# Optimization experiments

Measured on AMD Instinct MI355X. Metric: run time of the kernel, lower is better.

Reference implementation:

```python
import jax, jax.numpy as jnp
import numpy as np

H, C, HID, L, NF, B = 4, 128, 128, 3, 5, 32  # heads, per-head dim, hidden, layers, node feats, graphs
LN_EPS = 1e-5


def setup_inputs() -> dict:
    key = jax.random.key(0)
    ks = jax.random.split(key, 12)
    N, E = 10000, 160000
    x = jax.random.normal(ks[0], (N, NF), dtype=jnp.float32)
    edge_index = jax.random.randint(ks[1], (2, E), 0, N, dtype=jnp.int64)
    batch = jnp.sort(jax.random.randint(ks[2], (N,), 0, B, dtype=jnp.int64))
    s = 0.1
    return {
        "x": x,
        "edge_index": edge_index,
        "batch": batch,
        "node_W": jax.random.normal(ks[3], (NF, HID), dtype=jnp.float32) * s,
        "node_b": jnp.zeros((HID,), dtype=jnp.float32),
        "Ws": jax.random.normal(ks[4], (L, HID, H * C), dtype=jnp.float32) * s,
        "att_srcs": jax.random.normal(ks[5], (L, H, C), dtype=jnp.float32) * s,
        "att_dsts": jax.random.normal(ks[6], (L, H, C), dtype=jnp.float32) * s,
        "biases": jnp.zeros((L, HID), dtype=jnp.float32),
        "ln_gs": jnp.ones((L, HID), dtype=jnp.float32),
        "ln_bs": jnp.zeros((L, HID), dtype=jnp.float32),
    }


def _layer_norm(x, g, b):
    mu = jnp.mean(x, axis=-1, keepdims=True)
    var = jnp.mean(jnp.square(x - mu), axis=-1, keepdims=True)
    return (x - mu) * jax.lax.rsqrt(var + LN_EPS) * g + b


def _gat_layer(x, W, att_src, att_dst, bias, src, dst, N):
    # x: [N, HID]; PyG GATConv, heads=H, concat=False (mean over heads)
    h = (x @ W).reshape(N, H, C)                       # [N,H,C]
    a_src = jnp.sum(h * att_src, axis=-1)              # [N,H]
    a_dst = jnp.sum(h * att_dst, axis=-1)              # [N,H]
    e = jax.nn.leaky_relu(a_src[src] + a_dst[dst], 0.2)  # [E,H]
    # edge-softmax over destination neighborhoods (numerically stable)
    m = jax.ops.segment_max(e, dst, num_segments=N)
    ex = jnp.exp(e - m[dst])
    denom = jax.ops.segment_sum(ex, dst, num_segments=N)
    alpha = ex / (denom[dst] + 1e-16)                  # [E,H]
    msg = h[src] * alpha[:, :, None]                   # [E,H,C]
    out = jax.ops.segment_sum(msg, dst, num_segments=N)  # [N,H,C]
    return out.mean(axis=1) + bias                     # concat=False -> head mean


def reference(x, edge_index, batch, node_W, node_b, Ws, att_srcs, att_dsts,
              biases, ln_gs, ln_bs):
    N = x.shape[0]
    loop = jnp.arange(N, dtype=edge_index.dtype)
    src = jnp.concatenate([edge_index[0], loop])       # PyG adds self-loops
    dst = jnp.concatenate([edge_index[1], loop])

    h = jax.nn.relu(x @ node_W + node_b)               # [N,HID]
    for l in range(L):
        h_new = _gat_layer(h, Ws[l], att_srcs[l], att_dsts[l], biases[l], src, dst, N)
        h_new = _layer_norm(h_new, ln_gs[l], ln_bs[l])
        h = jax.nn.relu(h_new) + h                     # residual; dropout is identity in eval

    # global mean pool over graphs
    sums = jax.ops.segment_sum(h, batch, num_segments=B)
    cnts = jax.ops.segment_sum(jnp.ones((N, 1), h.dtype), batch, num_segments=B)
    graph_emb = sums / jnp.maximum(cnts, 1.0)
    return h, graph_emb
```

## Files before the change

### kernel.cpp

```cpp
#include <hip/hip_runtime.h>
#include <math.h>

#define N_NODES 10000
#define N_EDGES 160000
#define E2 (N_EDGES + N_NODES)
#define HIDDEN 128
#define NHEAD 4
#define NB 32
#define LN_EPS 1e-5f

typedef __attribute__((ext_vector_type(8))) short bf16x8;
typedef __attribute__((ext_vector_type(4))) float f32x4;

__device__ __forceinline__ unsigned short f2bf(float f) {
    unsigned int u = __float_as_uint(f);
    u += 0x7fffu + ((u >> 16) & 1u);
    return (unsigned short)(u >> 16);
}
__device__ __forceinline__ float bf2f_lo(unsigned int u) { return __uint_as_float(u << 16); }
__device__ __forceinline__ float bf2f_hi(unsigned int u) { return __uint_as_float(u & 0xffff0000u); }

__global__ void k_init(int* counts, int* gstart, int* gend, float* gout) {
    int i = blockIdx.x * blockDim.x + threadIdx.x;
    if (i < N_NODES) counts[i] = 1;
    if (i < NB) { gstart[i] = N_NODES; gend[i] = 0; }
    if (i < NB * HIDDEN) gout[i] = 0.f;
}

__global__ void k_hist(const int* __restrict__ ei, int* counts) {
    int e = blockIdx.x * blockDim.x + threadIdx.x;
    if (e < N_EDGES) atomicAdd(&counts[ei[N_EDGES + e]], 1);
}

__global__ void k_scan(const int* __restrict__ counts, int* rowptr, int* cursor) {
    __shared__ int sums[1024];
    int t = threadIdx.x;
    const int per = 10;
    int base = t * per;
    int loc[per];
    int s = 0;
    for (int i = 0; i < per; i++) {
        int idx = base + i;
        int v = (idx < N_NODES) ? counts[idx] : 0;
        loc[i] = s; s += v;
    }
    sums[t] = s;
    __syncthreads();
    for (int off = 1; off < 1024; off <<= 1) {
        int v = (t >= off) ? sums[t - off] : 0;
        __syncthreads();
        sums[t] += v;
        __syncthreads();
    }
    int prefix = (t > 0) ? sums[t - 1] : 0;
    for (int i = 0; i < per; i++) {
        int idx = base + i;
        if (idx < N_NODES) { int r = prefix + loc[i]; rowptr[idx] = r; cursor[idx] = r; }
    }
    if (t == 1023) rowptr[N_NODES] = sums[1023];
}

__global__ void k_scatter(const int* __restrict__ ei, int* cursor, int* csr_src) {
    int e = blockIdx.x * blockDim.x + threadIdx.x;
    if (e < N_EDGES) {
        int s = ei[e], d = ei[N_EDGES + e];
        int pos = atomicAdd(&cursor[d], 1);
        csr_src[pos] = s;
    } else if (e < E2) {
        int n = e - N_EDGES;
        int pos = atomicAdd(&cursor[n], 1);
        csr_src[pos] = n;
    }
}

__global__ void k_bounds(const int* __restrict__ batch, int* gstart, int* gend) {
    int n = blockIdx.x * blockDim.x + threadIdx.x;
    if (n >= N_NODES) return;
    int b = batch[n];
    if (n == 0 || batch[n - 1] != b) gstart[b] = n;
    if (n == N_NODES - 1 || batch[n + 1] != b) gend[b] = n + 1;
}

__global__ void k_convB(const float* __restrict__ Ws, unsigned short* __restrict__ Btb) {
    int t = blockIdx.x * blockDim.x + threadIdx.x;
    if (t >= 3 * 512 * 128) return;
    int l = t >> 16, rem = t & 65535;
    int n = rem >> 7, k = rem & 127;
    Btb[t] = f2bf(Ws[l * 65536 + k * 512 + n]);
}

__global__ void k_input(const float* __restrict__ x, const float* __restrict__ W,
                        const float* __restrict__ b, float* __restrict__ h,
                        unsigned short* __restrict__ hb) {
    int t = blockIdx.x * blockDim.x + threadIdx.x;
    if (t >= N_NODES * HIDDEN) return;
    int n = t >> 7, c = t & 127;
    float s = b[c];
    #pragma unroll
    for (int k = 0; k < 5; k++) s += x[n * 5 + k] * W[k * HIDDEN + c];
    float r = fmaxf(s, 0.f);
    h[t] = r;
    hb[t] = f2bf(r);
}

__global__ __launch_bounds__(256) void k_gemm(const unsigned short* __restrict__ Ab,
                                              const unsigned short* __restrict__ Bt,
                                              unsigned short* __restrict__ Cb) {
    int wave = threadIdx.x >> 6, lane = threadIdx.x & 63;
    int q = lane >> 4, u = lane & 15;
    int mbase = blockIdx.y * 64 + wave * 16;
    int nbase = blockIdx.x * 64;
    int arow = mbase + u;
    if (arow > N_NODES - 1) arow = N_NODES - 1;
    bf16x8 a[4];
    #pragma unroll
    for (int k0 = 0; k0 < 4; k0++)
        a[k0] = *(const bf16x8*)(Ab + (size_t)arow * 128 + k0 * 32 + q * 8);
    f32x4 acc[4];
    #pragma unroll
    for (int nb = 0; nb < 4; nb++) acc[nb] = (f32x4){0.f, 0.f, 0.f, 0.f};
    #pragma unroll
    for (int nb = 0; nb < 4; nb++) {
        const unsigned short* bp = Bt + (size_t)(nbase + nb * 16 + u) * 128 + q * 8;
        #pragma unroll
        for (int k0 = 0; k0 < 4; k0++) {
            bf16x8 bfr = *(const bf16x8*)(bp + k0 * 32);
            acc[nb] = __builtin_amdgcn_mfma_f32_16x16x32_bf16(a[k0], bfr, acc[nb], 0, 0, 0);
        }
    }
    #pragma unroll
    for (int nb = 0; nb < 4; nb++) {
        int col = nbase + nb * 16 + u;
        #pragma unroll
        for (int r = 0; r < 4; r++) {
            int row = mbase + q * 4 + r;
            if (row < N_NODES) Cb[(size_t)row * 512 + col] = f2bf(acc[nb][r]);
        }
    }
}

__global__ void k_att(const unsigned int* __restrict__ hb32,
                      const float* __restrict__ ws,
                      const float* __restrict__ wd, float* __restrict__ a_src,
                      float* __restrict__ a_dst) {
    int widx = blockIdx.x * 4 + (threadIdx.x >> 6);
    int lane = threadIdx.x & 63;
    if (widx >= N_NODES * NHEAD) return;
    int n = widx >> 2, h = widx & 3;
    unsigned int u = hb32[(size_t)n * 256 + h * 64 + lane];
    float v0 = bf2f_lo(u), v1 = bf2f_hi(u);
    int c = 2 * lane;
    float s = v0 * ws[h * 128 + c] + v1 * ws[h * 128 + c + 1];
    float d = v0 * wd[h * 128 + c] + v1 * wd[h * 128 + c + 1];
    #pragma unroll
    for (int o = 32; o > 0; o >>= 1) { s += __shfl_down(s, o); d += __shfl_down(d, o); }
    if (lane == 0) { a_src[widx] = s; a_dst[widx] = d; }
}

__global__ __launch_bounds__(256) void k_agg(const uint4* __restrict__ hb4,
                                             const int* __restrict__ rowptr,
                                             const int* __restrict__ csr,
                                             const float* __restrict__ a_src,
                                             const float* __restrict__ a_dst,
                                             const float* __restrict__ bias,
                                             const float* __restrict__ lng,
                                             const float* __restrict__ lnb,
                                             float* __restrict__ h,
                                             unsigned short* __restrict__ hbn) {
    int wave = threadIdx.x >> 6;
    int lane = threadIdx.x & 63;
    int n = blockIdx.x * 4 + wave;
    if (n >= N_NODES) return;
    int hl = lane >> 4;
    int pos = lane & 15;
    int off = rowptr[n];
    int deg = rowptr[n + 1] - off;
    float adn = a_dst[n * 4 + hl];
    float m = -INFINITY, denom = 0.f;
    float o[8] = {};
    for (int base = 0; base < deg; base += 64) {
        int cnt = min(64, deg - base);
        int s = (lane < cnt) ? csr[off + base + lane] : 0;
        for (int i = 0; i < cnt; i++) {
            int si = __shfl(s, i);
            float t = a_src[si * 4 + hl] + adn;
            float e = t > 0.f ? t : 0.2f * t;
            float nm = fmaxf(m, e);
            float sc = __expf(m - nm);
            float p = __expf(e - nm);
            denom = denom * sc + p;
            uint4 u = hb4[(size_t)si * 64 + lane];
            o[0] = o[0] * sc + p * bf2f_lo(u.x);
            o[1] = o[1] * sc + p * bf2f_hi(u.x);
            o[2] = o[2] * sc + p * bf2f_lo(u.y);
            o[3] = o[3] * sc + p * bf2f_hi(u.y);
            o[4] = o[4] * sc + p * bf2f_lo(u.z);
            o[5] = o[5] * sc + p * bf2f_hi(u.z);
            o[6] = o[6] * sc + p * bf2f_lo(u.w);
            o[7] = o[7] * sc + p * bf2f_hi(u.w);
            m = nm;
        }
    }
    float inv = 1.f / (denom + 1e-16f);
    #pragma unroll
    for (int k = 0; k < 8; k++) o[k] *= inv;
    #pragma unroll
    for (int k = 0; k < 8; k++) {
        o[k] += __shfl_xor(o[k], 16);
        o[k] += __shfl_xor(o[k], 32);
    }
    float v[8], sv = 0.f, sq = 0.f;
    #pragma unroll
    for (int k = 0; k < 8; k++) {
        float b = bias[8 * pos + k];
        v[k] = 0.25f * o[k] + b;
        sv += v[k]; sq += v[k] * v[k];
    }
    #pragma unroll
    for (int d = 8; d > 0; d >>= 1) {
        sv += __shfl_xor(sv, d);
        sq += __shfl_xor(sq, d);
    }
    float mu = sv * (1.f / 128.f);
    float var = sq * (1.f / 128.f) - mu * mu;
    float rs = rsqrtf(var + LN_EPS);
    if (hl == 0) {
        float* hrow = h + (size_t)n * 128 + 8 * pos;
        float4 old0 = *(const float4*)(hrow);
        float4 old1 = *(const float4*)(hrow + 4);
        float r[8];
        #pragma unroll
        for (int k = 0; k < 8; k++) {
            float y = (v[k] - mu) * rs * lng[8 * pos + k] + lnb[8 * pos + k];
            r[k] = fmaxf(y, 0.f);
        }
        float w[8] = {r[0] + old0.x, r[1] + old0.y, r[2] + old0.z, r[3] + old0.w,
                      r[4] + old1.x, r[5] + old1.y, r[6] + old1.z, r[7] + old1.w};
        *(float4*)(hrow) = make_float4(w[0], w[1], w[2], w[3]);
        *(float4*)(hrow + 4) = make_float4(w[4], w[5], w[6], w[7]);
        ushort4 p0, p1;
        p0.x = f2bf(w[0]); p0.y = f2bf(w[1]); p0.z = f2bf(w[2]); p0.w = f2bf(w[3]);
        p1.x = f2bf(w[4]); p1.y = f2bf(w[5]); p1.z = f2bf(w[6]); p1.w = f2bf(w[7]);
        unsigned short* hbrow = hbn + (size_t)n * 128 + 8 * pos;
        *(ushort4*)(hbrow) = p0;
        *(ushort4*)(hbrow + 4) = p1;
    }
}

#define POOL_CHUNK 32
__global__ __launch_bounds__(128) void k_pool_sum(const float* __restrict__ h,
                                                  const int* __restrict__ batch,
                                                  float* __restrict__ gout) {
    int n0 = blockIdx.x * POOL_CHUNK;
    int c = threadIdx.x;
    int nend = min(n0 + POOL_CHUNK, N_NODES);
    if (n0 >= N_NODES) return;
    int cur = batch[n0];
    float acc = 0.f;
    for (int n = n0; n < nend; n++) {
        int b = batch[n];
        if (b != cur) {
            atomicAdd(&gout[cur * HIDDEN + c], acc);
            acc = 0.f; cur = b;
        }
        acc += h[(size_t)n * HIDDEN + c];
    }
    atomicAdd(&gout[cur * HIDDEN + c], acc);
}

__global__ void k_pool_div(const int* __restrict__ gstart, const int* __restrict__ gend,
                           float* __restrict__ gout) {
    int b = blockIdx.x, c = threadIdx.x;
    int cnt = gend[b] - gstart[b];
    gout[b * HIDDEN + c] *= 1.f / (float)max(cnt, 1);
}

extern "C" void kernel_launch(void* const* d_in, const int* in_sizes, int n_in,
                              void* d_out, int out_size, void* d_ws, size_t ws_size,
                              hipStream_t stream) {
    const float* x      = (const float*)d_in[0];
    const int*   ei     = (const int*)d_in[1];
    const int*   batch  = (const int*)d_in[2];
    const float* node_W = (const float*)d_in[3];
    const float* node_b = (const float*)d_in[4];
    const float* Ws     = (const float*)d_in[5];
    const float* att_s  = (const float*)d_in[6];
    const float* att_d  = (const float*)d_in[7];
    const float* biases = (const float*)d_in[8];
    const float* ln_g   = (const float*)d_in[9];
    const float* ln_b   = (const float*)d_in[10];

    float* out = (float*)d_out;
    float* h = out;
    float* gout = out + (size_t)N_NODES * HIDDEN;

    char* w = (char*)d_ws;
    auto carve = [&](size_t bytes) {
        void* p = (void*)w;
        w += (bytes + 255) & ~(size_t)255;
        return p;
    };
    int* rowptr  = (int*)carve((N_NODES + 1) * sizeof(int));
    int* cursor  = (int*)carve(N_NODES * sizeof(int));
    int* counts  = (int*)carve(N_NODES * sizeof(int));
    int* csr     = (int*)carve(E2 * sizeof(int));
    int* gstart  = (int*)carve(NB * sizeof(int));
    int* gend    = (int*)carve(NB * sizeof(int));
    float* a_src = (float*)carve((size_t)N_NODES * NHEAD * sizeof(float));
    float* a_dst = (float*)carve((size_t)N_NODES * NHEAD * sizeof(float));
    unsigned short* hb  = (unsigned short*)carve((size_t)N_NODES * 512 * sizeof(unsigned short));
    unsigned short* hbx = (unsigned short*)carve((size_t)N_NODES * HIDDEN * sizeof(unsigned short));
    unsigned short* Btb = (unsigned short*)carve((size_t)3 * 512 * 128 * sizeof(unsigned short));

    k_init<<<(N_NODES + 255) / 256, 256, 0, stream>>>(counts, gstart, gend, gout);
    k_hist<<<(N_EDGES + 255) / 256, 256, 0, stream>>>(ei, counts);
    k_scan<<<1, 1024, 0, stream>>>(counts, rowptr, cursor);
    k_scatter<<<(E2 + 255) / 256, 256, 0, stream>>>(ei, cursor, csr);
    k_bounds<<<(N_NODES + 255) / 256, 256, 0, stream>>>(batch, gstart, gend);
    k_convB<<<(3 * 512 * 128 + 255) / 256, 256, 0, stream>>>(Ws, Btb);
    k_input<<<(N_NODES * HIDDEN + 255) / 256, 256, 0, stream>>>(x, node_W, node_b, h, hbx);

    for (int l = 0; l < 3; l++) {
        k_gemm<<<dim3(8, (N_NODES + 63) / 64), 256, 0, stream>>>(
            hbx, Btb + (size_t)l * 512 * 128, hb);
        k_att<<<N_NODES, 256, 0, stream>>>((const unsigned int*)hb,
                                           att_s + l * NHEAD * 128,
                                           att_d + l * NHEAD * 128, a_src, a_dst);
        k_agg<<<(N_NODES + 3) / 4, 256, 0, stream>>>((const uint4*)hb, rowptr, csr,
                                           a_src, a_dst,
                                           biases + l * HIDDEN, ln_g + l * HIDDEN,
                                           ln_b + l * HIDDEN, h, hbx);
    }
    k_pool_sum<<<(N_NODES + POOL_CHUNK - 1) / POOL_CHUNK, 128, 0, stream>>>(h, batch, gout);
    k_pool_div<<<NB, HIDDEN, 0, stream>>>(gstart, gend, gout);
}
```

Baseline: 290.3 us.

## Fuse preprocessing kernels, attention logits into GEMM epilogue, and pool division

Merges the input projection, degree histogram, weight conversion and graph-bounds kernels into one launch, with counts zeroed by memset and the self-loop +1 moved into the scan. Computes the per-head attention source and destination logits directly from the GEMM accumulators. Each block now covers one head over 32 rows, with shuffle and shared-memory reduction, which removes the separate k_att pass that re-read the projected features. Folds the mean-pool division into the pooling atomics. gstart/gend are no longer initialised, so a graph with no nodes would read undefined bounds.

Result: faster. 272.6 us (-6.1%).

```diff
diff --git a/kernel.cpp b/kernel.cpp
--- a/kernel.cpp
+++ b/kernel.cpp
@@ -9,6 +9,12 @@
 #define NB 32
 #define LN_EPS 1e-5f
 
+#define T_INPUT (N_NODES * HIDDEN)
+#define T_HIST  (T_INPUT + N_EDGES)
+#define T_CONV  (T_HIST + 3 * 512 * 128)
+#define T_BOUND (T_CONV + N_NODES)
+#define T_TOTAL T_BOUND
+
 typedef __attribute__((ext_vector_type(8))) short bf16x8;
 typedef __attribute__((ext_vector_type(4))) float f32x4;
 
@@ -20,16 +26,39 @@
 __device__ __forceinline__ float bf2f_lo(unsigned int u) { return __uint_as_float(u << 16); }
 __device__ __forceinline__ float bf2f_hi(unsigned int u) { return __uint_as_float(u & 0xffff0000u); }
 
-__global__ void k_init(int* counts, int* gstart, int* gend, float* gout) {
-    int i = blockIdx.x * blockDim.x + threadIdx.x;
-    if (i < N_NODES) counts[i] = 1;
-    if (i < NB) { gstart[i] = N_NODES; gend[i] = 0; }
-    if (i < NB * HIDDEN) gout[i] = 0.f;
-}
-
-__global__ void k_hist(const int* __restrict__ ei, int* counts) {
-    int e = blockIdx.x * blockDim.x + threadIdx.x;
-    if (e < N_EDGES) atomicAdd(&counts[ei[N_EDGES + e]], 1);
+__global__ __launch_bounds__(256) void k_pre(const float* __restrict__ x,
+                                             const float* __restrict__ W,
+                                             const float* __restrict__ b,
+                                             const int* __restrict__ ei,
+                                             const int* __restrict__ batch,
+                                             const float* __restrict__ Ws,
+                                             float* __restrict__ h,
+                                             unsigned short* __restrict__ hb,
+                                             int* counts, int* gstart, int* gend,
+                                             unsigned short* __restrict__ Btb) {
+    int t = blockIdx.x * blockDim.x + threadIdx.x;
+    if (t < T_INPUT) {
+        int n = t >> 7, c = t & 127;
+        float s = b[c];
+        #pragma unroll
+        for (int k = 0; k < 5; k++) s += x[n * 5 + k] * W[k * HIDDEN + c];
+        float r = fmaxf(s, 0.f);
+        h[t] = r;
+        hb[t] = f2bf(r);
+    } else if (t < T_HIST) {
+        int e = t - T_INPUT;
+        atomicAdd(&counts[ei[N_EDGES + e]], 1);
+    } else if (t < T_CONV) {
+        int i = t - T_HIST;
+        int l = i >> 16, rem = i & 65535;
+        int n = rem >> 7, k = rem & 127;
+        Btb[i] = f2bf(Ws[l * 65536 + k * 512 + n]);
+    } else if (t < T_BOUND) {
+        int n = t - T_CONV;
+        int bb = batch[n];
+        if (n == 0 || batch[n - 1] != bb) gstart[bb] = n;
+        if (n == N_NODES - 1 || batch[n + 1] != bb) gend[bb] = n + 1;
+    }
 }
 
 __global__ void k_scan(const int* __restrict__ counts, int* rowptr, int* cursor) {
@@ -41,7 +70,7 @@
     int s = 0;
     for (int i = 0; i < per; i++) {
         int idx = base + i;
-        int v = (idx < N_NODES) ? counts[idx] : 0;
+        int v = (idx < N_NODES) ? counts[idx] + 1 : 0;
         loc[i] = s; s += v;
     }
     sums[t] = s;
@@ -73,43 +102,19 @@
     }
 }
 
-__global__ void k_bounds(const int* __restrict__ batch, int* gstart, int* gend) {
-    int n = blockIdx.x * blockDim.x + threadIdx.x;
-    if (n >= N_NODES) return;
-    int b = batch[n];
-    if (n == 0 || batch[n - 1] != b) gstart[b] = n;
-    if (n == N_NODES - 1 || batch[n + 1] != b) gend[b] = n + 1;
-}
-
-__global__ void k_convB(const float* __restrict__ Ws, unsigned short* __restrict__ Btb) {
-    int t = blockIdx.x * blockDim.x + threadIdx.x;
-    if (t >= 3 * 512 * 128) return;
-    int l = t >> 16, rem = t & 65535;
-    int n = rem >> 7, k = rem & 127;
-    Btb[t] = f2bf(Ws[l * 65536 + k * 512 + n]);
-}
-
-__global__ void k_input(const float* __restrict__ x, const float* __restrict__ W,
-                        const float* __restrict__ b, float* __restrict__ h,
-                        unsigned short* __restrict__ hb) {
-    int t = blockIdx.x * blockDim.x + threadIdx.x;
-    if (t >= N_NODES * HIDDEN) return;
-    int n = t >> 7, c = t & 127;
-    float s = b[c];
-    #pragma unroll
-    for (int k = 0; k < 5; k++) s += x[n * 5 + k] * W[k * HIDDEN + c];
-    float r = fmaxf(s, 0.f);
-    h[t] = r;
-    hb[t] = f2bf(r);
-}
-
-__global__ __launch_bounds__(256) void k_gemm(const unsigned short* __restrict__ Ab,
-                                              const unsigned short* __restrict__ Bt,
-                                              unsigned short* __restrict__ Cb) {
+__global__ __launch_bounds__(256) void k_gemm_att(const unsigned short* __restrict__ Ab,
+                                                  const unsigned short* __restrict__ Bt,
+                                                  const float* __restrict__ ws,
+                                                  const float* __restrict__ wd,
+                                                  unsigned short* __restrict__ Cb,
+                                                  float* __restrict__ a_src,
+                                                  float* __restrict__ a_dst) {
     int wave = threadIdx.x >> 6, lane = threadIdx.x & 63;
     int q = lane >> 4, u = lane & 15;
-    int mbase = blockIdx.y * 64 + wave * 16;
-    int nbase = blockIdx.x * 64;
+    int h = blockIdx.x;
+    int rowgrp = wave & 1, colhalf = wave >> 1;
+    int mbase = blockIdx.y * 32 + rowgrp * 16;
+    int colbase = h * 128 + colhalf * 64;
     int arow = mbase + u;
     if (arow > N_NODES - 1) arow = N_NODES - 1;
     bf16x8 a[4];
@@ -121,7 +126,7 @@
     for (int nb = 0; nb < 4; nb++) acc[nb] = (f32x4){0.f, 0.f, 0.f, 0.f};
     #pragma unroll
     for (int nb = 0; nb < 4; nb++) {
-        const unsigned short* bp = Bt + (size_t)(nbase + nb * 16 + u) * 128 + q * 8;
+        const unsigned short* bp = Bt + (size_t)(colbase + nb * 16 + u) * 128 + q * 8;
         #pragma unroll
         for (int k0 = 0; k0 < 4; k0++) {
             bf16x8 bfr = *(const bf16x8*)(bp + k0 * 32);
@@ -130,31 +135,45 @@
     }
     #pragma unroll
     for (int nb = 0; nb < 4; nb++) {
-        int col = nbase + nb * 16 + u;
+        int col = colbase + nb * 16 + u;
         #pragma unroll
         for (int r = 0; r < 4; r++) {
             int row = mbase + q * 4 + r;
             if (row < N_NODES) Cb[(size_t)row * 512 + col] = f2bf(acc[nb][r]);
         }
     }
-}
-
-__global__ void k_att(const unsigned int* __restrict__ hb32,
-                      const float* __restrict__ ws,
-                      const float* __restrict__ wd, float* __restrict__ a_src,
-                      float* __restrict__ a_dst) {
-    int widx = blockIdx.x * 4 + (threadIdx.x >> 6);
-    int lane = threadIdx.x & 63;
-    if (widx >= N_NODES * NHEAD) return;
-    int n = widx >> 2, h = widx & 3;
-    unsigned int u = hb32[(size_t)n * 256 + h * 64 + lane];
-    float v0 = bf2f_lo(u), v1 = bf2f_hi(u);
-    int c = 2 * lane;
-    float s = v0 * ws[h * 128 + c] + v1 * ws[h * 128 + c + 1];
-    float d = v0 * wd[h * 128 + c] + v1 * wd[h * 128 + c + 1];
-    #pragma unroll
-    for (int o = 32; o > 0; o >>= 1) { s += __shfl_down(s, o); d += __shfl_down(d, o); }
-    if (lane == 0) { a_src[widx] = s; a_dst[widx] = d; }
+    float ps[4] = {}, pd[4] = {};
+    #pragma unroll
+    for (int nb = 0; nb < 4; nb++) {
+        int cl = colhalf * 64 + nb * 16 + u;
+        float wsv = ws[h * 128 + cl], wdv = wd[h * 128 + cl];
+        #pragma unroll
+        for (int r = 0; r < 4; r++) { ps[r] += acc[nb][r] * wsv; pd[r] += acc[nb][r] * wdv; }
+    }
+    #pragma unroll
+    for (int d = 1; d < 16; d <<= 1) {
+        #pragma unroll
+        for (int r = 0; r < 4; r++) {
+            ps[r] += __shfl_xor(ps[r], d);
+            pd[r] += __shfl_xor(pd[r], d);
+        }
+    }
+    __shared__ float ls[2][2][16], ldd[2][2][16];
+    if (u == 0) {
+        #pragma unroll
+        for (int r = 0; r < 4; r++) {
+            ls[rowgrp][colhalf][q * 4 + r] = ps[r];
+            ldd[rowgrp][colhalf][q * 4 + r] = pd[r];
+        }
+    }
+    __syncthreads();
+    if (colhalf == 0 && lane < 16) {
+        int row = mbase + lane;
+        if (row < N_NODES) {
+            a_src[row * 4 + h] = ls[rowgrp][0][lane] + ls[rowgrp][1][lane];
+            a_dst[row * 4 + h] = ldd[rowgrp][0][lane] + ldd[rowgrp][1][lane];
+        }
+    }
 }
 
 __global__ __launch_bounds__(256) void k_agg(const uint4* __restrict__ hb4,
@@ -250,6 +269,8 @@
 #define POOL_CHUNK 32
 __global__ __launch_bounds__(128) void k_pool_sum(const float* __restrict__ h,
                                                   const int* __restrict__ batch,
+                                                  const int* __restrict__ gstart,
+                                                  const int* __restrict__ gend,
                                                   float* __restrict__ gout) {
     int n0 = blockIdx.x * POOL_CHUNK;
     int c = threadIdx.x;
@@ -260,19 +281,14 @@
     for (int n = n0; n < nend; n++) {
         int b = batch[n];
         if (b != cur) {
-            atomicAdd(&gout[cur * HIDDEN + c], acc);
+            float inv = 1.f / (float)max(gend[cur] - gstart[cur], 1);
+            atomicAdd(&gout[cur * HIDDEN + c], acc * inv);
             acc = 0.f; cur = b;
         }
         acc += h[(size_t)n * HIDDEN + c];
     }
-    atomicAdd(&gout[cur * HIDDEN + c], acc);
-}
-
-__global__ void k_pool_div(const int* __restrict__ gstart, const int* __restrict__ gend,
-                           float* __restrict__ gout) {
-    int b = blockIdx.x, c = threadIdx.x;
-    int cnt = gend[b] - gstart[b];
-    gout[b * HIDDEN + c] *= 1.f / (float)max(cnt, 1);
+    float inv = 1.f / (float)max(gend[cur] - gstart[cur], 1);
+    atomicAdd(&gout[cur * HIDDEN + c], acc * inv);
 }
 
 extern "C" void kernel_launch(void* const* d_in, const int* in_sizes, int n_in,
@@ -312,25 +328,24 @@
     unsigned short* hbx = (unsigned short*)carve((size_t)N_NODES * HIDDEN * sizeof(unsigned short));
     unsigned short* Btb = (unsigned short*)carve((size_t)3 * 512 * 128 * sizeof(unsigned short));
 
-    k_init<<<(N_NODES + 255) / 256, 256, 0, stream>>>(counts, gstart, gend, gout);
-    k_hist<<<(N_EDGES + 255) / 256, 256, 0, stream>>>(ei, counts);
+    hipMemsetAsync(counts, 0, N_NODES * sizeof(int), stream);
+    hipMemsetAsync(gout, 0, NB * HIDDEN * sizeof(float), stream);
+
+    k_pre<<<(T_TOTAL + 255) / 256, 256, 0, stream>>>(x, node_W, node_b, ei, batch, Ws,
+                                                     h, hbx, counts, gstart, gend, Btb);
     k_scan<<<1, 1024, 0, stream>>>(counts, rowptr, cursor);
     k_scatter<<<(E2 + 255) / 256, 256, 0, stream>>>(ei, cursor, csr);
-    k_bounds<<<(N_NODES + 255) / 256, 256, 0, stream>>>(batch, gstart, gend);
-    k_convB<<<(3 * 512 * 128 + 255) / 256, 256, 0, stream>>>(Ws, Btb);
-    k_input<<<(N_NODES * HIDDEN + 255) / 256, 256, 0, stream>>>(x, node_W, node_b, h, hbx);
 
     for (int l = 0; l < 3; l++) {
-        k_gemm<<<dim3(8, (N_NODES + 63) / 64), 256, 0, stream>>>(
-            hbx, Btb + (size_t)l * 512 * 128, hb);
-        k_att<<<N_NODES, 256, 0, stream>>>((const unsigned int*)hb,
-                                           att_s + l * NHEAD * 128,
-                                           att_d + l * NHEAD * 128, a_src, a_dst);
+        k_gemm_att<<<dim3(4, (N_NODES + 31) / 32), 256, 0, stream>>>(
+            hbx, Btb + (size_t)l * 512 * 128,
+            att_s + l * NHEAD * 128, att_d + l * NHEAD * 128,
+            hb, a_src, a_dst);
         k_agg<<<(N_NODES + 3) / 4, 256, 0, stream>>>((const uint4*)hb, rowptr, csr,
                                            a_src, a_dst,
                                            biases + l * HIDDEN, ln_g + l * HIDDEN,
                                            ln_b + l * HIDDEN, h, hbx);
     }
-    k_pool_sum<<<(N_NODES + POOL_CHUNK - 1) / POOL_CHUNK, 128, 0, stream>>>(h, batch, gout);
-    k_pool_div<<<NB, HIDDEN, 0, stream>>>(gstart, gend, gout);
-}
+    k_pool_sum<<<(N_NODES + POOL_CHUNK - 1) / POOL_CHUNK, 128, 0, stream>>>(
+        h, batch, gstart, gend, gout);
+}
```
